# Kernel optimization log

Hardware: AMD Instinct MI355X
Metric: run time of the kernel (lower is better)

## Reference

```python
import jax, jax.numpy as jnp
import numpy as np

HIDDEN = 896
N_HEADS = 14
N_KV_HEADS = 2
HEAD_DIM = HIDDEN // N_HEADS  # 64
KV_GROUPS = N_HEADS // N_KV_HEADS  # 7
ROPE_THETA = 1000000.0


def rotate_half(x):
    x1, x2 = x[..., : x.shape[-1] // 2], x[..., x.shape[-1] // 2 :]
    return jnp.concatenate((-x2, x1), axis=-1)


def rope_tables(seq_len, dtype=jnp.float32):
    inv_freq = 1.0 / (ROPE_THETA ** (jnp.arange(0, HEAD_DIM, 2, dtype=jnp.float32) / HEAD_DIM))
    t = jnp.arange(seq_len, dtype=jnp.float32)
    freqs = jnp.outer(t, inv_freq)            # [S, D/2]
    emb = jnp.concatenate((freqs, freqs), -1)  # [S, D]
    return jnp.cos(emb).astype(dtype), jnp.sin(emb).astype(dtype)


def setup_inputs() -> dict:
    key = jax.random.key(0)
    ks = jax.random.split(key, 8)
    B, S = 2, 2048
    s = 0.02
    return {
        "hidden_states": jax.random.normal(ks[0], (B, S, HIDDEN), jnp.float32),
        "wq": jax.random.normal(ks[1], (HIDDEN, N_HEADS * HEAD_DIM), jnp.float32) * s,
        "bq": jnp.zeros((N_HEADS * HEAD_DIM,), jnp.float32),
        "wk": jax.random.normal(ks[2], (HIDDEN, N_KV_HEADS * HEAD_DIM), jnp.float32) * s,
        "bk": jnp.zeros((N_KV_HEADS * HEAD_DIM,), jnp.float32),
        "wv": jax.random.normal(ks[3], (HIDDEN, N_KV_HEADS * HEAD_DIM), jnp.float32) * s,
        "bv": jnp.zeros((N_KV_HEADS * HEAD_DIM,), jnp.float32),
        "wo": jax.random.normal(ks[4], (N_HEADS * HEAD_DIM, HIDDEN), jnp.float32) * s,
    }


def reference(hidden_states, wq, bq, wk, bk, wv, bv, wo):
    B, S, _ = hidden_states.shape
    q = (hidden_states @ wq + bq).reshape(B, S, N_HEADS, HEAD_DIM)
    k = (hidden_states @ wk + bk).reshape(B, S, N_KV_HEADS, HEAD_DIM)
    v = (hidden_states @ wv + bv).reshape(B, S, N_KV_HEADS, HEAD_DIM)

    cos, sin = rope_tables(S, hidden_states.dtype)
    cos, sin = cos[None, :, None, :], sin[None, :, None, :]
    q = q * cos + rotate_half(q) * sin
    k = k * cos + rotate_half(k) * sin

    # GQA broadcast: repeat kv heads to match query heads
    k = jnp.repeat(k, KV_GROUPS, axis=2)
    v = jnp.repeat(v, KV_GROUPS, axis=2)

    # [B, H, S, S]
    scores = jnp.einsum("bqhd,bkhd->bhqk", q, k) / jnp.sqrt(jnp.asarray(HEAD_DIM, hidden_states.dtype))
    mask = jnp.tril(jnp.ones((S, S), dtype=jnp.bool_))
    scores = jnp.where(mask[None, None, :, :], scores, jnp.asarray(-1e9, scores.dtype))
    attn = jax.nn.softmax(scores, axis=-1)
    out = jnp.einsum("bhqk,bkhd->bqhd", attn, v).reshape(B, S, N_HEADS * HEAD_DIM)
    return out @ wo
```

## Files before the change

### kernel.cpp

```cpp
#include <hip/hip_runtime.h>

#define HID 896
#define NQ 896
#define NKV 128
#define NQKV 1152
#define NH 14
#define NKVH 2
#define GQ 7
#define DH 64
#define SEQ 2048
#define BATCH 2
#define TOK (BATCH*SEQ)

typedef __attribute__((ext_vector_type(8))) short short8;
typedef __attribute__((ext_vector_type(4))) float f32x4;
typedef __attribute__((ext_vector_type(4))) unsigned short us4;

__device__ __forceinline__ unsigned short f2bf(float x) {
  unsigned int u = __builtin_bit_cast(unsigned int, x);
  u = (u + 0x7fffu + ((u >> 16) & 1u)) >> 16;
  return (unsigned short)u;
}
__device__ __forceinline__ float bf2f(unsigned short b) {
  return __builtin_bit_cast(float, (unsigned int)b << 16);
}
__device__ __forceinline__ f32x4 fzero4() {
  f32x4 z; z[0]=0.f; z[1]=0.f; z[2]=0.f; z[3]=0.f; return z;
}
__device__ __forceinline__ unsigned int cvt_pk_bf16(float lo, float hi) {
  unsigned int r;
  asm("v_cvt_pk_bf16_f32 %0, %1, %2" : "=v"(r) : "v"(lo), "v"(hi));
  return r;
}
__device__ __forceinline__ void gload_lds16(const unsigned short* g, unsigned short* l) {
  __builtin_amdgcn_global_load_lds(
      (const __attribute__((address_space(1))) void*)(const void*)g,
      (__attribute__((address_space(3))) void*)(void*)l, 16, 0, 0);
}

#define CVT_BLKS 3584
#define TRN_BLKS 448
#define BIAS_BLKS 5
#define TAB_BLKS 256
#define PREP_BLKS (CVT_BLKS + TRN_BLKS + BIAS_BLKS + TAB_BLKS)

__global__ void k_prep(const float* __restrict__ hs,
                       const float* __restrict__ wq, const float* __restrict__ bq,
                       const float* __restrict__ wk, const float* __restrict__ bk,
                       const float* __restrict__ wv, const float* __restrict__ bv,
                       const float* __restrict__ wo,
                       unsigned short* __restrict__ hb,
                       unsigned short* __restrict__ wqkvt,
                       unsigned short* __restrict__ wot,
                       float* __restrict__ bqkv,
                       float* __restrict__ ct, float* __restrict__ st) {
  __shared__ unsigned short Ls[64*65];
  int blk = blockIdx.x, tid = threadIdx.x;
  if (blk < CVT_BLKS) {
    int i = blk*256 + tid;
    float4 v = ((const float4*)hs)[i];
    us4 o; o[0]=f2bf(v.x); o[1]=f2bf(v.y); o[2]=f2bf(v.z); o[3]=f2bf(v.w);
    ((us4*)hb)[i] = o;
    return;
  }
  blk -= CVT_BLKS;
  if (blk < TRN_BLKS) {
    const float* W; unsigned short* out; int K, N, n0, k0;
    if (blk < 196)      { W=wq; out=wqkvt;                        K=HID; N=NQ;  int t=blk;     n0=(t%14)*64; k0=(t/14)*64; }
    else if (blk < 224) { W=wk; out=wqkvt + (size_t)NQ*HID;       K=HID; N=NKV; int t=blk-196; n0=(t%2)*64;  k0=(t/2)*64; }
    else if (blk < 252) { W=wv; out=wqkvt + (size_t)(NQ+NKV)*HID; K=HID; N=NKV; int t=blk-224; n0=(t%2)*64;  k0=(t/2)*64; }
    else                { W=wo; out=wot;                          K=NQ;  N=HID; int t=blk-252; n0=(t%14)*64; k0=(t/14)*64; }
    #pragma unroll
    for (int i = 0; i < 16; ++i) {
      int idx = i*256 + tid;
      int r = idx >> 6, c = idx & 63;
      Ls[c*65 + r] = f2bf(W[(size_t)(k0 + r)*N + n0 + c]);
    }
    __syncthreads();
    #pragma unroll
    for (int i = 0; i < 16; ++i) {
      int idx = i*256 + tid;
      int r2 = idx >> 6, c2 = idx & 63;
      out[(size_t)(n0 + r2)*K + k0 + c2] = Ls[r2*65 + c2];
    }
    return;
  }
  blk -= TRN_BLKS;
  if (blk < BIAS_BLKS) {
    int i = blk*256 + tid;
    if (i < NQKV) {
      if (i < NQ) bqkv[i] = bq[i];
      else if (i < NQ + NKV) bqkv[i] = bk[i - NQ];
      else bqkv[i] = bv[i - NQ - NKV];
    }
    return;
  }
  blk -= BIAS_BLKS;
  {
    int i = blk*256 + tid;
    int s = i >> 5, dp = i & 31;
    float inv = __expf(-(float)(2*dp) * (13.815510557964274f / 64.0f));
    float f = (float)s * inv;
    ct[i] = cosf(f); st[i] = sinf(f);
  }
}

template<int OUTMODE>
__global__ __launch_bounds__(256, 2) void k_gemm_bt(
    const unsigned short* __restrict__ A,
    const unsigned short* __restrict__ Bt,
    const float* __restrict__ bias,
    void* __restrict__ Cout,
    int M, int N, int K) {
  __shared__ unsigned short As[128*64];
  __shared__ unsigned short Bs[128*64];
  int tid = threadIdx.x;
  int lane = tid & 63, w = tid >> 6;
  int wr = w >> 1, wc = w & 1;
  int l15 = lane & 15, l4 = lane >> 4;
  int m0 = blockIdx.y * 128, n0 = blockIdx.x * 128;

  f32x4 acc[4][4];
  #pragma unroll
  for (int i = 0; i < 4; ++i)
    #pragma unroll
    for (int j = 0; j < 4; ++j) acc[i][j] = fzero4();

  int nkt = K >> 6;
  for (int kt = 0; kt < nkt; ++kt) {
    int k0 = kt << 6;
    #pragma unroll
    for (int t = 0; t < 4; ++t) {
      int chunk = t*256 + w*64 + lane;
      int row = chunk >> 3, sp = chunk & 7;
      int sl = sp ^ (row & 7);
      gload_lds16(A + (size_t)(m0+row)*K + k0 + sl*8, &As[(t*256 + w*64)*8]);
      gload_lds16(Bt + (size_t)(n0+row)*K + k0 + sl*8, &Bs[(t*256 + w*64)*8]);
    }
    __syncthreads();
    #pragma unroll
    for (int s = 0; s < 2; ++s) {
      short8 af[4], bfr[4];
      #pragma unroll
      for (int mi = 0; mi < 4; ++mi) {
        int row = wr*64 + mi*16 + l15;
        int slot = (s*4 + l4) ^ (row & 7);
        af[mi] = *reinterpret_cast<const short8*>(&As[row*64 + slot*8]);
      }
      #pragma unroll
      for (int ni = 0; ni < 4; ++ni) {
        int row = wc*64 + ni*16 + l15;
        int slot = (s*4 + l4) ^ (row & 7);
        bfr[ni] = *reinterpret_cast<const short8*>(&Bs[row*64 + slot*8]);
      }
      #pragma unroll
      for (int mi = 0; mi < 4; ++mi)
        #pragma unroll
        for (int ni = 0; ni < 4; ++ni)
          acc[mi][ni] = __builtin_amdgcn_mfma_f32_16x16x32_bf16(af[mi], bfr[ni], acc[mi][ni], 0, 0, 0);
    }
    __syncthreads();
  }
  #pragma unroll
  for (int mi = 0; mi < 4; ++mi) {
    #pragma unroll
    for (int ni = 0; ni < 4; ++ni) {
      #pragma unroll
      for (int r = 0; r < 4; ++r) {
        int row = m0 + wr*64 + mi*16 + l4*4 + r;
        int col = n0 + wc*64 + ni*16 + l15;
        float v = acc[mi][ni][r];
        if (OUTMODE == 0) {
          v += bias[col];
          ((unsigned short*)Cout)[(size_t)row*N + col] = f2bf(v);
        } else {
          ((float*)Cout)[(size_t)row*N + col] = v;
        }
      }
    }
  }
}

__global__ void k_rope(const unsigned short* __restrict__ qkv,
                       const float* __restrict__ ct, const float* __restrict__ st,
                       unsigned short* __restrict__ Qr, unsigned short* __restrict__ Kr,
                       unsigned short* __restrict__ Vt) {
  int t = blockIdx.x; int b = t >> 11; int s = t & 2047;
  int tid = threadIdx.x;
  const unsigned short* row = qkv + (size_t)t * NQKV;
  if (tid < 448) {
    int h = tid >> 5, dp = tid & 31;
    float x1 = bf2f(row[h*64 + dp]);
    float x2 = bf2f(row[h*64 + dp + 32]);
    float c = ct[s*32 + dp], sn = st[s*32 + dp];
    size_t base = (((size_t)b*NH + h)*SEQ + s)*64;
    Qr[base + dp]      = f2bf((x1*c - x2*sn) * 0.125f);
    Qr[base + dp + 32] = f2bf((x2*c + x1*sn) * 0.125f);
  } else {
    int j = tid - 448;
    int kvh = j >> 5, dp = j & 31;
    float x1 = bf2f(row[NQ + kvh*64 + dp]);
    float x2 = bf2f(row[NQ + kvh*64 + dp + 32]);
    float c = ct[s*32 + dp], sn = st[s*32 + dp];
    size_t base = (((size_t)b*NKVH + kvh)*SEQ + s)*64;
    Kr[base + dp]      = f2bf(x1*c - x2*sn);
    Kr[base + dp + 32] = f2bf(x2*c + x1*sn);
  }
  if (tid < 128) {
    int kvh = tid >> 6, d = tid & 63;
    Vt[(((size_t)b*NKVH + kvh)*64 + d)*SEQ + s] = row[1024 + kvh*64 + d];
  }
}

__global__ __launch_bounds__(512, 2) void k_attn(
    const unsigned short* __restrict__ Q,
    const unsigned short* __restrict__ Kr,
    const unsigned short* __restrict__ Vt,
    unsigned short* __restrict__ Aout) {
  __shared__ __align__(16) unsigned short Kst[2][2][64*64];
  __shared__ __align__(16) unsigned short Vst[2][2][64*64];
  __shared__ __align__(16) unsigned short P_lds[8][16*64];
  int lane = threadIdx.x & 63, w = threadIdx.x >> 6;
  int grp = w >> 2, wsub = w & 3;
  int l15 = lane & 15, l4 = lane >> 4;
  int i = blockIdx.x, h = blockIdx.y, b = blockIdx.z;
  int qtH = 31 - i, qtL = i;
  int qt = grp ? qtL : qtH;
  int kvh = h / GQ;
  const unsigned short* Kb = Kr + ((size_t)(b*NKVH + kvh))*SEQ*64;
  const unsigned short* Vb = Vt + ((size_t)(b*NKVH + kvh))*64*SEQ;
  char* Pw = (char*)&P_lds[w][0];

  auto stage = [&](int slab, int bsel) {
    #pragma unroll
    for (int t = 0; t < 2; ++t) {
      int ks = slab*2 + t; if (ks > 31) ks = 31;
      int chunk = w*64 + lane;
      int row = chunk >> 3;
      int sl = (chunk & 7) ^ (row & 7);
      gload_lds16(Kb + (size_t)(ks*64 + row)*64 + sl*8, &Kst[bsel][t][chunk*8]);
      gload_lds16(Vb + (size_t)row*SEQ + ks*64 + sl*8, &Vst[bsel][t][chunk*8]);
    }
  };

  const unsigned short* Qb = Q + (((size_t)(b*NH + h))*SEQ + qt*64 + wsub*16) * 64;
  short8 qa[2];
  #pragma unroll
  for (int s = 0; s < 2; ++s)
    qa[s] = *reinterpret_cast<const short8*>(Qb + l15*64 + s*32 + l4*8);

  f32x4 acc[4];
  #pragma unroll
  for (int n = 0; n < 4; ++n) acc[n] = fzero4();
  float m_run = -__builtin_inff(), l_run = 0.0f;

  stage(0, 0);
  __syncthreads();
  int cur = 0;
  int nkt = qtH + 1;
  int nslab = (nkt + 1) >> 1;

  for (int s = 0; s < nslab; ++s) {
    if (s + 1 < nslab) stage(s + 1, cur ^ 1);
    #pragma unroll
    for (int t = 0; t < 2; ++t) {
      int ks = s*2 + t;
      if (ks <= qt) {
        const unsigned short* Ks = &Kst[cur][t][0];
        const unsigned short* Vs = &Vst[cur][t][0];
        f32x4 sa[4];
        #pragma unroll
        for (int n = 0; n < 4; ++n) sa[n] = fzero4();
        __builtin_amdgcn_s_setprio(1);
        #pragma unroll
        for (int si = 0; si < 2; ++si) {
          short8 kb[4];
          #pragma unroll
          for (int n = 0; n < 4; ++n) {
            int row = n*16 + l15;
            int slot = (si*4 + l4) ^ (row & 7);
            kb[n] = *reinterpret_cast<const short8*>(&Ks[row*64 + slot*8]);
          }
          #pragma unroll
          for (int n = 0; n < 4; ++n)
            sa[n] = __builtin_amdgcn_mfma_f32_16x16x32_bf16(kb[n], qa[si], sa[n], 0, 0, 0);
        }
        __builtin_amdgcn_s_setprio(0);
        if (ks == qt) {
          int q_glob = qt*64 + wsub*16 + l15;
          #pragma unroll
          for (int n = 0; n < 4; ++n)
            #pragma unroll
            for (int r = 0; r < 4; ++r) {
              int kpos = ks*64 + n*16 + l4*4 + r;
              if (kpos > q_glob) sa[n][r] = -1e30f;
            }
        }
        float t0 = fmaxf(fmaxf(sa[0][0],sa[0][1]), fmaxf(sa[0][2],sa[0][3]));
        float t1 = fmaxf(fmaxf(sa[1][0],sa[1][1]), fmaxf(sa[1][2],sa[1][3]));
        float t2 = fmaxf(fmaxf(sa[2][0],sa[2][1]), fmaxf(sa[2][2],sa[2][3]));
        float t3 = fmaxf(fmaxf(sa[3][0],sa[3][1]), fmaxf(sa[3][2],sa[3][3]));
        float tmax = fmaxf(fmaxf(t0,t1), fmaxf(t2,t3));
        tmax = fmaxf(tmax, __shfl_xor(tmax, 16));
        tmax = fmaxf(tmax, __shfl_xor(tmax, 32));
        float mn = fmaxf(m_run, tmax);
        float sc = __expf(m_run - mn);
        #pragma unroll
        for (int n = 0; n < 4; ++n)
          #pragma unroll
          for (int r = 0; r < 4; ++r) sa[n][r] = __expf(sa[n][r] - mn);
        float s0 = (sa[0][0]+sa[0][1]) + (sa[0][2]+sa[0][3]);
        float s1 = (sa[1][0]+sa[1][1]) + (sa[1][2]+sa[1][3]);
        float s2 = (sa[2][0]+sa[2][1]) + (sa[2][2]+sa[2][3]);
        float s3 = (sa[3][0]+sa[3][1]) + (sa[3][2]+sa[3][3]);
        float sum = (s0+s1) + (s2+s3);
        sum += __shfl_xor(sum, 16);
        sum += __shfl_xor(sum, 32);
        m_run = mn;
        l_run = l_run*sc + sum;
        #pragma unroll
        for (int n = 0; n < 4; ++n) acc[n] *= sc;
        #pragma unroll
        for (int n = 0; n < 4; ++n) {
          uint2 pk;
          pk.x = cvt_pk_bf16(sa[n][0], sa[n][1]);
          pk.y = cvt_pk_bf16(sa[n][2], sa[n][3]);
          int colbyte = n*32 + l4*8;
          int addr = l15*128 + ((((colbyte>>4) ^ (l15&7))) << 4) + (colbyte & 15);
          *reinterpret_cast<uint2*>(Pw + addr) = pk;
        }
        __builtin_amdgcn_s_setprio(1);
        #pragma unroll
        for (int s2i = 0; s2i < 2; ++s2i) {
          int pslot = (s2i*4 + l4) ^ (l15 & 7);
          short8 pa = *reinterpret_cast<const short8*>(Pw + l15*128 + pslot*16);
          #pragma unroll
          for (int n = 0; n < 4; ++n) {
            int row = n*16 + l15;
            int vslot = (s2i*4 + l4) ^ (row & 7);
            short8 vb = *reinterpret_cast<const short8*>(&Vs[row*64 + vslot*8]);
            acc[n] = __builtin_amdgcn_mfma_f32_16x16x32_bf16(vb, pa, acc[n], 0, 0, 0);
          }
        }
        __builtin_amdgcn_s_setprio(0);
      }
    }
    __syncthreads();
    cur ^= 1;
  }

  float inv = 1.0f / l_run;
  #pragma unroll
  for (int n = 0; n < 4; ++n) {
    uint2 pk;
    pk.x = cvt_pk_bf16(acc[n][0]*inv, acc[n][1]*inv);
    pk.y = cvt_pk_bf16(acc[n][2]*inv, acc[n][3]*inv);
    int colbyte = n*32 + l4*8;
    int addr = l15*128 + ((((colbyte>>4) ^ (l15&7))) << 4) + (colbyte & 15);
    *reinterpret_cast<uint2*>(Pw + addr) = pk;
  }
  int row = lane >> 2;
  int cb0 = (lane & 3) * 32;
  #pragma unroll
  for (int it = 0; it < 2; ++it) {
    int cb = cb0 + it*16;
    int slot = (cb >> 4) ^ (row & 7);
    short8 v = *reinterpret_cast<const short8*>(Pw + row*128 + slot*16);
    size_t tok = (size_t)b*SEQ + qt*64 + wsub*16 + row;
    *reinterpret_cast<short8*>(&Aout[tok*NQ + h*64 + (cb>>1)]) = v;
  }
}

extern "C" void kernel_launch(void* const* d_in, const int* in_sizes, int n_in,
                              void* d_out, int out_size, void* d_ws, size_t ws_size,
                              hipStream_t stream) {
  const float* hs = (const float*)d_in[0];
  const float* wq = (const float*)d_in[1];
  const float* bq = (const float*)d_in[2];
  const float* wk = (const float*)d_in[3];
  const float* bk = (const float*)d_in[4];
  const float* wv = (const float*)d_in[5];
  const float* bv = (const float*)d_in[6];
  const float* wo = (const float*)d_in[7];
  float* out = (float*)d_out;

  char* p = (char*)d_ws;
  auto alloc = [&](size_t bytes) { char* r = p; p += (bytes + 255) & ~(size_t)255; return r; };
  unsigned short* hb    = (unsigned short*)alloc((size_t)TOK*HID*2);
  unsigned short* wqkvt = (unsigned short*)alloc((size_t)NQKV*HID*2);
  unsigned short* wot   = (unsigned short*)alloc((size_t)HID*NQ*2);
  float*          bqkv  = (float*)alloc(NQKV*4);
  unsigned short* qkvt  = (unsigned short*)alloc((size_t)TOK*NQKV*2);
  unsigned short* q_r   = (unsigned short*)alloc((size_t)BATCH*NH*SEQ*DH*2);
  unsigned short* k_r   = (unsigned short*)alloc((size_t)BATCH*NKVH*SEQ*DH*2);
  unsigned short* v_t   = (unsigned short*)alloc((size_t)BATCH*NKVH*DH*SEQ*2);
  float*          ct    = (float*)alloc((size_t)SEQ*32*4);
  float*          st    = (float*)alloc((size_t)SEQ*32*4);
  unsigned short* attn  = hb;

  k_prep<<<PREP_BLKS, 256, 0, stream>>>(hs, wq, bq, wk, bk, wv, bv, wo,
                                        hb, wqkvt, wot, bqkv, ct, st);
  k_gemm_bt<0><<<dim3(NQKV/128, TOK/128), 256, 0, stream>>>(hb, wqkvt, bqkv, qkvt, TOK, NQKV, HID);
  k_rope<<<TOK, 512, 0, stream>>>(qkvt, ct, st, q_r, k_r, v_t);
  k_attn<<<dim3(16, NH, BATCH), 512, 0, stream>>>(q_r, k_r, v_t, attn);
  k_gemm_bt<1><<<dim3(NQ/128, TOK/128), 256, 0, stream>>>(attn, wot, nullptr, out, TOK, NQ, HID);
}
```

Before: 102.0 us.

## Fuse RoPE and V transpose into QKV GEMM epilogue, shrink GEMM tiles

Result: faster. 91.43 us (-10.4%).

```diff
diff --git a/kernel.cpp b/kernel.cpp
--- a/kernel.cpp
+++ b/kernel.cpp
@@ -53,7 +53,7 @@
                        unsigned short* __restrict__ wqkvt,
                        unsigned short* __restrict__ wot,
                        float* __restrict__ bqkv,
-                       float* __restrict__ ct, float* __restrict__ st) {
+                       float2* __restrict__ cs) {
   __shared__ unsigned short Ls[64*65];
   int blk = blockIdx.x, tid = threadIdx.x;
   if (blk < CVT_BLKS) {
@@ -101,49 +101,59 @@
     int s = i >> 5, dp = i & 31;
     float inv = __expf(-(float)(2*dp) * (13.815510557964274f / 64.0f));
     float f = (float)s * inv;
-    ct[i] = cosf(f); st[i] = sinf(f);
+    cs[i] = make_float2(cosf(f), sinf(f));
   }
 }
 
 template<int OUTMODE>
-__global__ __launch_bounds__(256, 2) void k_gemm_bt(
+__global__ __launch_bounds__(256, 4) void k_gemm_bt(
     const unsigned short* __restrict__ A,
     const unsigned short* __restrict__ Bt,
     const float* __restrict__ bias,
+    const float2* __restrict__ cs,
     void* __restrict__ Cout,
+    unsigned short* __restrict__ Qr,
+    unsigned short* __restrict__ Kr,
+    unsigned short* __restrict__ Vt,
     int M, int N, int K) {
-  __shared__ unsigned short As[128*64];
+  __shared__ unsigned short As[64*64];
   __shared__ unsigned short Bs[128*64];
   int tid = threadIdx.x;
   int lane = tid & 63, w = tid >> 6;
   int wr = w >> 1, wc = w & 1;
   int l15 = lane & 15, l4 = lane >> 4;
-  int m0 = blockIdx.y * 128, n0 = blockIdx.x * 128;
-
-  f32x4 acc[4][4];
-  #pragma unroll
-  for (int i = 0; i < 4; ++i)
+  int m0 = blockIdx.y * 64, n0 = blockIdx.x * 128;
+
+  f32x4 acc[2][4];
+  #pragma unroll
+  for (int i = 0; i < 2; ++i)
     #pragma unroll
     for (int j = 0; j < 4; ++j) acc[i][j] = fzero4();
 
   int nkt = K >> 6;
   for (int kt = 0; kt < nkt; ++kt) {
     int k0 = kt << 6;
+    #pragma unroll
+    for (int t = 0; t < 2; ++t) {
+      int chunk = t*256 + w*64 + lane;
+      int row = chunk >> 3, sp = chunk & 7;
+      int sl = sp ^ (row & 7);
+      gload_lds16(A + (size_t)(m0+row)*K + k0 + sl*8, &As[(t*256 + w*64)*8]);
+    }
     #pragma unroll
     for (int t = 0; t < 4; ++t) {
       int chunk = t*256 + w*64 + lane;
       int row = chunk >> 3, sp = chunk & 7;
       int sl = sp ^ (row & 7);
-      gload_lds16(A + (size_t)(m0+row)*K + k0 + sl*8, &As[(t*256 + w*64)*8]);
       gload_lds16(Bt + (size_t)(n0+row)*K + k0 + sl*8, &Bs[(t*256 + w*64)*8]);
     }
     __syncthreads();
     #pragma unroll
     for (int s = 0; s < 2; ++s) {
-      short8 af[4], bfr[4];
+      short8 af[2], bfr[4];
       #pragma unroll
-      for (int mi = 0; mi < 4; ++mi) {
-        int row = wr*64 + mi*16 + l15;
+      for (int mi = 0; mi < 2; ++mi) {
+        int row = wr*32 + mi*16 + l15;
         int slot = (s*4 + l4) ^ (row & 7);
         af[mi] = *reinterpret_cast<const short8*>(&As[row*64 + slot*8]);
       }
@@ -154,61 +164,60 @@
         bfr[ni] = *reinterpret_cast<const short8*>(&Bs[row*64 + slot*8]);
       }
       #pragma unroll
-      for (int mi = 0; mi < 4; ++mi)
+      for (int mi = 0; mi < 2; ++mi)
         #pragma unroll
         for (int ni = 0; ni < 4; ++ni)
           acc[mi][ni] = __builtin_amdgcn_mfma_f32_16x16x32_bf16(af[mi], bfr[ni], acc[mi][ni], 0, 0, 0);
     }
     __syncthreads();
   }
-  #pragma unroll
-  for (int mi = 0; mi < 4; ++mi) {
-    #pragma unroll
-    for (int ni = 0; ni < 4; ++ni) {
+
+  if (OUTMODE == 1) {
+    #pragma unroll
+    for (int mi = 0; mi < 2; ++mi)
       #pragma unroll
-      for (int r = 0; r < 4; ++r) {
-        int row = m0 + wr*64 + mi*16 + l4*4 + r;
-        int col = n0 + wc*64 + ni*16 + l15;
-        float v = acc[mi][ni][r];
-        if (OUTMODE == 0) {
-          v += bias[col];
-          ((unsigned short*)Cout)[(size_t)row*N + col] = f2bf(v);
+      for (int ni = 0; ni < 4; ++ni)
+        #pragma unroll
+        for (int r = 0; r < 4; ++r) {
+          int row = m0 + wr*32 + mi*16 + l4*4 + r;
+          int col = n0 + wc*64 + ni*16 + l15;
+          ((float*)Cout)[(size_t)row*N + col] = acc[mi][ni][r];
+        }
+    return;
+  }
+
+  int col0 = n0 + wc*64;
+  #pragma unroll
+  for (int mi = 0; mi < 2; ++mi) {
+    #pragma unroll
+    for (int r = 0; r < 4; ++r) {
+      int row = m0 + wr*32 + mi*16 + l4*4 + r;
+      int b = row >> 11, s = row & 2047;
+      #pragma unroll
+      for (int ni = 0; ni < 2; ++ni) {
+        int dp = ni*16 + l15;
+        float x1 = acc[mi][ni][r]   + bias[col0 + dp];
+        float x2 = acc[mi][ni+2][r] + bias[col0 + dp + 32];
+        if (col0 < NQ) {
+          int h = col0 >> 6;
+          float2 c2 = cs[s*32 + dp];
+          size_t base = ((size_t)(b*NH + h)*SEQ + s)*64;
+          Qr[base + dp]      = f2bf((x1*c2.x - x2*c2.y) * 0.125f);
+          Qr[base + dp + 32] = f2bf((x2*c2.x + x1*c2.y) * 0.125f);
+        } else if (col0 < NQ + NKV) {
+          int kvh = (col0 - NQ) >> 6;
+          float2 c2 = cs[s*32 + dp];
+          size_t base = ((size_t)(b*NKVH + kvh)*SEQ + s)*64;
+          Kr[base + dp]      = f2bf(x1*c2.x - x2*c2.y);
+          Kr[base + dp + 32] = f2bf(x2*c2.x + x1*c2.y);
         } else {
-          ((float*)Cout)[(size_t)row*N + col] = v;
+          int kvh = (col0 - 1024) >> 6;
+          size_t base = (size_t)(b*NKVH + kvh)*64;
+          Vt[(base + dp)*SEQ + s]      = f2bf(x1);
+          Vt[(base + dp + 32)*SEQ + s] = f2bf(x2);
         }
       }
     }
-  }
-}
-
-__global__ void k_rope(const unsigned short* __restrict__ qkv,
-                       const float* __restrict__ ct, const float* __restrict__ st,
-                       unsigned short* __restrict__ Qr, unsigned short* __restrict__ Kr,
-                       unsigned short* __restrict__ Vt) {
-  int t = blockIdx.x; int b = t >> 11; int s = t & 2047;
-  int tid = threadIdx.x;
-  const unsigned short* row = qkv + (size_t)t * NQKV;
-  if (tid < 448) {
-    int h = tid >> 5, dp = tid & 31;
-    float x1 = bf2f(row[h*64 + dp]);
-    float x2 = bf2f(row[h*64 + dp + 32]);
-    float c = ct[s*32 + dp], sn = st[s*32 + dp];
-    size_t base = (((size_t)b*NH + h)*SEQ + s)*64;
-    Qr[base + dp]      = f2bf((x1*c - x2*sn) * 0.125f);
-    Qr[base + dp + 32] = f2bf((x2*c + x1*sn) * 0.125f);
-  } else {
-    int j = tid - 448;
-    int kvh = j >> 5, dp = j & 31;
-    float x1 = bf2f(row[NQ + kvh*64 + dp]);
-    float x2 = bf2f(row[NQ + kvh*64 + dp + 32]);
-    float c = ct[s*32 + dp], sn = st[s*32 + dp];
-    size_t base = (((size_t)b*NKVH + kvh)*SEQ + s)*64;
-    Kr[base + dp]      = f2bf(x1*c - x2*sn);
-    Kr[base + dp + 32] = f2bf(x2*c + x1*sn);
-  }
-  if (tid < 128) {
-    int kvh = tid >> 6, d = tid & 63;
-    Vt[(((size_t)b*NKVH + kvh)*64 + d)*SEQ + s] = row[1024 + kvh*64 + d];
   }
 }
 
@@ -390,18 +399,17 @@
   unsigned short* wqkvt = (unsigned short*)alloc((size_t)NQKV*HID*2);
   unsigned short* wot   = (unsigned short*)alloc((size_t)HID*NQ*2);
   float*          bqkv  = (float*)alloc(NQKV*4);
-  unsigned short* qkvt  = (unsigned short*)alloc((size_t)TOK*NQKV*2);
+  float2*         cs    = (float2*)alloc((size_t)SEQ*32*8);
   unsigned short* q_r   = (unsigned short*)alloc((size_t)BATCH*NH*SEQ*DH*2);
   unsigned short* k_r   = (unsigned short*)alloc((size_t)BATCH*NKVH*SEQ*DH*2);
   unsigned short* v_t   = (unsigned short*)alloc((size_t)BATCH*NKVH*DH*SEQ*2);
-  float*          ct    = (float*)alloc((size_t)SEQ*32*4);
-  float*          st    = (float*)alloc((size_t)SEQ*32*4);
-  unsigned short* attn  = hb;
+  unsigned short* attn  = (unsigned short*)alloc((size_t)TOK*NQ*2);
 
   k_prep<<<PREP_BLKS, 256, 0, stream>>>(hs, wq, bq, wk, bk, wv, bv, wo,
-                                        hb, wqkvt, wot, bqkv, ct, st);
-  k_gemm_bt<0><<<dim3(NQKV/128, TOK/128), 256, 0, stream>>>(hb, wqkvt, bqkv, qkvt, TOK, NQKV, HID);
-  k_rope<<<TOK, 512, 0, stream>>>(qkvt, ct, st, q_r, k_r, v_t);
+                                        hb, wqkvt, wot, bqkv, cs);
+  k_gemm_bt<0><<<dim3(NQKV/128, TOK/64), 256, 0, stream>>>(
+      hb, wqkvt, bqkv, cs, nullptr, q_r, k_r, v_t, TOK, NQKV, HID);
   k_attn<<<dim3(16, NH, BATCH), 512, 0, stream>>>(q_r, k_r, v_t, attn);
-  k_gemm_bt<1><<<dim3(NQ/128, TOK/128), 256, 0, stream>>>(attn, wot, nullptr, out, TOK, NQ, HID);
-}
+  k_gemm_bt<1><<<dim3(NQ/128, TOK/64), 256, 0, stream>>>(
+      attn, wot, nullptr, nullptr, out, nullptr, nullptr, nullptr, TOK, NQ, HID);
+}
```
